# Optimization experiments

Hardware: AMD Instinct MI355X
Metric: run time of the kernel (lower is better)

The kernel has to match this reference:

```python
import jax, jax.numpy as jnp
from jax import lax
import numpy as np

GROUPS = 4


def _grid_sample_border(img, gx, gy):
    # img: [Bg, Cg, H, W]; gx, gy: [Bg, H, W] normalized grid in [-1, 1]
    # Replicates F.grid_sample(mode='bilinear', align_corners=False, padding_mode='border')
    Bg, Cg, H, W = img.shape
    ix = jnp.clip(((gx + 1.0) * W - 1.0) * 0.5, 0.0, W - 1.0)
    iy = jnp.clip(((gy + 1.0) * H - 1.0) * 0.5, 0.0, H - 1.0)
    x0 = jnp.floor(ix)
    y0 = jnp.floor(iy)
    wx = ix - x0
    wy = iy - y0
    x0i = x0.astype(jnp.int32)
    y0i = y0.astype(jnp.int32)
    x1i = jnp.minimum(x0i + 1, W - 1)
    y1i = jnp.minimum(y0i + 1, H - 1)

    def one(im, x0i, x1i, y0i, y1i, wx, wy):
        v00 = im[:, y0i, x0i]
        v01 = im[:, y0i, x1i]
        v10 = im[:, y1i, x0i]
        v11 = im[:, y1i, x1i]
        return (v00 * (1 - wx) * (1 - wy) + v01 * wx * (1 - wy)
                + v10 * (1 - wx) * wy + v11 * wx * wy)

    return jax.vmap(one)(img, x0i, x1i, y0i, y1i, wx, wy)


def setup_inputs() -> dict:
    key = jax.random.key(0)
    ks = jax.random.split(key, 8)
    B, N, C = 8, 4096, 768
    x = jax.random.normal(ks[0], (B, N, C), dtype=jnp.float32)
    dw_w = jax.random.normal(ks[1], (C, 1, 3, 3), dtype=jnp.float32) * 0.1  # depthwise kernel
    dw_b = jax.random.normal(ks[2], (C,), dtype=jnp.float32) * 0.1
    off_w = jax.random.normal(ks[3], (2 * GROUPS, C), dtype=jnp.float32) * 0.001  # std=0.001 init
    off_b = jnp.zeros((2 * GROUPS,), dtype=jnp.float32)
    wt_w = jax.random.normal(ks[4], (2 * GROUPS, C), dtype=jnp.float32) * 0.02
    wt_b = jnp.zeros((2 * GROUPS,), dtype=jnp.float32)
    offset_list = jnp.zeros((1,), dtype=jnp.int32)
    return {"x": x, "dw_w": dw_w, "dw_b": dw_b, "off_w": off_w, "off_b": off_b,
            "wt_w": wt_w, "wt_b": wt_b, "offset_list": offset_list,
            "patch_h": 64, "patch_w": 64}


def reference(x, dw_w, dw_b, off_w, off_b, wt_w, wt_b, offset_list, patch_h, patch_w):
    B, N, C = x.shape
    H, W = int(patch_h), int(patch_w)
    xi = jnp.transpose(x, (0, 2, 1)).reshape(B, C, H, W)

    # offset head: depthwise 3x3 conv -> GELU -> 1x1 conv to 2*groups channels
    dw = lax.conv_general_dilated(xi, dw_w, (1, 1), ((1, 1), (1, 1)),
                                  dimension_numbers=("NCHW", "OIHW", "NCHW"),
                                  feature_group_count=C)
    dw = jax.nn.gelu(dw + dw_b[None, :, None, None], approximate=False)
    off = jnp.einsum("bchw,oc->bohw", dw, off_w) + off_b[None, :, None, None]

    # weight head: 1x1 conv -> sigmoid
    wt = jax.nn.sigmoid(jnp.einsum("bchw,oc->bohw", xi, wt_w) + wt_b[None, :, None, None])

    off = (off * wt).reshape(B, 2, GROUPS, H, W)
    # fixed cross-shaped shifts: x-comp [0,0,-1,+1], y-comp [-1,+1,0,0]
    shifts = jnp.array([[0.0, 0.0, -1.0, 1.0], [-1.0, 1.0, 0.0, 0.0]],
                       dtype=x.dtype).reshape(1, 2, GROUPS, 1, 1)
    off = off + shifts

    cx = (jnp.arange(W, dtype=x.dtype) + 0.5)[None, None, None, :]  # pixel-center x coords
    cy = (jnp.arange(H, dtype=x.dtype) + 0.5)[None, None, :, None]  # pixel-center y coords
    gx = 2.0 * (cx + off[:, 0]) / W - 1.0  # [B, GROUPS, H, W]
    gy = 2.0 * (cy + off[:, 1]) / H - 1.0

    img = xi.reshape(B * GROUPS, C // GROUPS, H, W)
    samp = _grid_sample_border(img, gx.reshape(B * GROUPS, H, W),
                               gy.reshape(B * GROUPS, H, W))
    out = samp.reshape(B, C, N)
    return jnp.transpose(out, (0, 2, 1))  # [B, N, C]
```

## Files before the change

### kernel.cpp

```cpp
#include <hip/hip_runtime.h>
#include <math.h>

#define BB 8
#define CC 768
#define HH 64
#define WW 64
#define NN 4096
#define GG 4
#define NCHUNK 6
#define CHUNK 128

typedef __attribute__((ext_vector_type(8))) short short8;
typedef __attribute__((ext_vector_type(4))) float f32x4;

__device__ __forceinline__ unsigned short f2bf(float f) {
    union { float f; unsigned u; } v; v.f = f;
    unsigned r = v.u + 0x7FFFu + ((v.u >> 16) & 1u);
    return (unsigned short)(r >> 16);
}

__device__ __forceinline__ float gelu_fast(float v) {
    const float z = 1.5957691216f * v * fmaf(0.044715f, v * v, 1.0f);
    return __fdividef(v, 1.0f + __expf(-z));
}

__global__ __launch_bounds__(128, 4) void dq_conv_mfma(
    const float* __restrict__ x,
    const float* __restrict__ dw_w,
    const float* __restrict__ dw_b,
    const float* __restrict__ off_w,
    const float* __restrict__ wt_w,
    float* __restrict__ offpart)
{
    __shared__ unsigned short gl[16][144];
    __shared__ unsigned short xh[16][144];
    const int t = threadIdx.x;
    const int lane = t & 63, wv = t >> 6;
    const int xcd = blockIdx.x & 7;
    const int local = blockIdx.x >> 3;
    const int chunk = local % NCHUNK;
    const int r = xcd * (BB * HH / 8) + local / NCHUNK;
    const int h = r & (HH - 1);
    const int b = r >> 6;
    const int c = chunk * CHUNK + t;

    const int n = lane & 15, kg = lane >> 4;
    const float* wsrc = (wv == 0) ? off_w : wt_w;
    short8 bfrag[4];
#pragma unroll
    for (int kt = 0; kt < 4; ++kt) {
        const bool valid = (n < 8);
        const float* src = wsrc + (valid ? n : 0) * CC + chunk * CHUNK + kt * 32 + kg * 8;
        short8 bf;
#pragma unroll
        for (int j = 0; j < 8; ++j) {
            const float v = valid ? src[j] : 0.f;
            bf[j] = (short)f2bf(v);
        }
        bfrag[kt] = bf;
    }

    float w9[9];
#pragma unroll
    for (int j = 0; j < 9; ++j) w9[j] = dw_w[c * 9 + j];
    const float bias = dw_b[c];
    const bool tv = (h > 0), bv = (h < HH - 1);
    const float wt0 = tv ? w9[0] : 0.f, wt1 = tv ? w9[1] : 0.f, wt2 = tv ? w9[2] : 0.f;
    const float wb0 = bv ? w9[6] : 0.f, wb1 = bv ? w9[7] : 0.f, wb2 = bv ? w9[8] : 0.f;

    const float* base = x + (size_t)b * NN * CC + c;
    const float* rT = base + (size_t)((tv ? h - 1 : 0) * WW) * CC;
    const float* rM = base + (size_t)(h * WW) * CC;
    const float* rB = base + (size_t)((bv ? h + 1 : h) * WW) * CC;

    float cT[8], cM[8], cB[8], nT[8], nM[8], nB[8];
    float pT = 0.f, pM = 0.f, pB = 0.f;

#pragma unroll
    for (int j = 0; j < 8; ++j) {
        const size_t o = (size_t)j * CC;
        cT[j] = rT[o]; cM[j] = rM[o]; cB[j] = rB[o];
    }

#pragma unroll
    for (int q = 0; q < 4; ++q) {
#pragma unroll
        for (int hb = 0; hb < 2; ++hb) {
            const int wb = q * 2 + hb;
            if (wb < 7) {
#pragma unroll
                for (int j = 0; j < 8; ++j) {
                    const size_t o = (size_t)(wb * 8 + 8 + j) * CC;
                    nT[j] = rT[o]; nM[j] = rM[o]; nB[j] = rB[o];
                }
            } else {
#pragma unroll
                for (int j = 0; j < 8; ++j) { nT[j] = 0.f; nM[j] = 0.f; nB[j] = 0.f; }
            }
#pragma unroll
            for (int j = 0; j < 8; ++j) {
                const float lT = j ? cT[j - 1] : pT;
                const float lM = j ? cM[j - 1] : pM;
                const float lB = j ? cB[j - 1] : pB;
                const float rTv = (j == 7) ? nT[0] : cT[j + 1];
                const float rMv = (j == 7) ? nM[0] : cM[j + 1];
                const float rBv = (j == 7) ? nB[0] : cB[j + 1];
                const float conv = lT * wt0 + cT[j] * wt1 + rTv * wt2
                                 + lM * w9[3] + cM[j] * w9[4] + rMv * w9[5]
                                 + lB * wb0 + cB[j] * wb1 + rBv * wb2;
                const int colq = hb * 8 + j;
                gl[colq][t] = f2bf(gelu_fast(conv + bias));
                xh[colq][t] = f2bf(cM[j]);
            }
            pT = cT[7]; pM = cM[7]; pB = cB[7];
#pragma unroll
            for (int j = 0; j < 8; ++j) { cT[j] = nT[j]; cM[j] = nM[j]; cB[j] = nB[j]; }
        }

        __syncthreads();
        f32x4 acc = {0.f, 0.f, 0.f, 0.f};
        if (wv == 0) {
#pragma unroll
            for (int kt = 0; kt < 4; ++kt) {
                const short8 a = *(const short8*)&gl[n][kt * 32 + kg * 8];
                acc = __builtin_amdgcn_mfma_f32_16x16x32_bf16(a, bfrag[kt], acc, 0, 0, 0);
            }
        } else {
#pragma unroll
            for (int kt = 0; kt < 4; ++kt) {
                const short8 a = *(const short8*)&xh[n][kt * 32 + kg * 8];
                acc = __builtin_amdgcn_mfma_f32_16x16x32_bf16(a, bfrag[kt], acc, 0, 0, 0);
            }
        }
        if (n < 8) {
            const int plane = chunk * 16 + (wv ? 8 + n : n);
            const size_t gpos = (size_t)(b * NN) + h * WW + q * 16 + kg * 4;
            float4 st; st.x = acc[0]; st.y = acc[1]; st.z = acc[2]; st.w = acc[3];
            *(float4*)&offpart[(size_t)plane * (BB * NN) + gpos] = st;
        }
        if (q < 3) __syncthreads();
    }
}

__global__ __launch_bounds__(256) void dq_combine(
    const float* __restrict__ offpart,
    const float* __restrict__ off_b,
    const float* __restrict__ wt_b,
    float* __restrict__ ixiy)
{
    const int t = threadIdx.x;
    const int o = t >> 5;
    const int gpos = blockIdx.x * 32 + (t & 31);
    const int b = gpos >> 12;
    const int hw = gpos & 4095;
    const int h = hw >> 6, w = hw & 63;

    float so = 0.f, sw = 0.f;
#pragma unroll
    for (int ch = 0; ch < NCHUNK; ++ch) {
        so += offpart[((size_t)(ch * 16 + o)) * (BB * NN) + gpos];
        sw += offpart[((size_t)(ch * 16 + 8 + o)) * (BB * NN) + gpos];
    }
    const float sig = 1.f / (1.f + __expf(-(sw + wt_b[o])));
    const float val = (so + off_b[o]) * sig;

    if (o < 4) {
        const float shx = (o == 2) ? -1.f : ((o == 3) ? 1.f : 0.f);
        const float ix = fminf(fmaxf((float)w + val + shx, 0.f), (float)(WW - 1));
        ixiy[(b * GG + o) * NN + hw] = ix;
    } else {
        const int g = o - 4;
        const float shy = (g == 0) ? -1.f : ((g == 1) ? 1.f : 0.f);
        const float iy = fminf(fmaxf((float)h + val + shy, 0.f), (float)(HH - 1));
        ixiy[BB * GG * NN + (b * GG + g) * NN + hw] = iy;
    }
}

__global__ __launch_bounds__(192) void dq_sample_vec(
    const float* __restrict__ x,
    const float* __restrict__ ixiy,
    float* __restrict__ out)
{
    __shared__ float ixy[8];
    const int t = threadIdx.x;
    const int p = (blockIdx.x & 7) * (BB * NN / 8) + (blockIdx.x >> 3);
    const int b = p >> 12;
    const int hw = p & 4095;

    if (t < 8) {
        const int g = t & 3;
        const int plane = (t >> 2) * (BB * GG * NN);
        ixy[t] = ixiy[plane + (b * GG + g) * NN + hw];
    }
    __syncthreads();

    const int g = t / 48;
    const float ix = ixy[g], iy = ixy[4 + g];
    const float x0f = floorf(ix), y0f = floorf(iy);
    const float wx = ix - x0f, wy = iy - y0f;
    const int x0 = (int)x0f, y0 = (int)y0f;
    const int x1 = min(x0 + 1, WW - 1), y1 = min(y0 + 1, HH - 1);
    const int c4 = t * 4;
    const float* xb = x + (size_t)b * NN * CC;
    const float4 v00 = *(const float4*)(xb + (size_t)(y0 * WW + x0) * CC + c4);
    const float4 v01 = *(const float4*)(xb + (size_t)(y0 * WW + x1) * CC + c4);
    const float4 v10 = *(const float4*)(xb + (size_t)(y1 * WW + x0) * CC + c4);
    const float4 v11 = *(const float4*)(xb + (size_t)(y1 * WW + x1) * CC + c4);
    const float w00 = (1.f - wx) * (1.f - wy), w01 = wx * (1.f - wy);
    const float w10 = (1.f - wx) * wy,         w11 = wx * wy;
    float4 r;
    r.x = v00.x * w00 + v01.x * w01 + v10.x * w10 + v11.x * w11;
    r.y = v00.y * w00 + v01.y * w01 + v10.y * w10 + v11.y * w11;
    r.z = v00.z * w00 + v01.z * w01 + v10.z * w10 + v11.z * w11;
    r.w = v00.w * w00 + v01.w * w01 + v10.w * w10 + v11.w * w11;
    *(float4*)(out + (size_t)p * CC + c4) = r;
}

__global__ __launch_bounds__(256) void dqshift_offsets_kernel(
    const float* __restrict__ x, const float* __restrict__ dw_w,
    const float* __restrict__ dw_b, const float* __restrict__ off_w,
    const float* __restrict__ off_b, const float* __restrict__ wt_w,
    const float* __restrict__ wt_b, float* __restrict__ ixiy)
{
    const int wave = threadIdx.x >> 6;
    const int lane = threadIdx.x & 63;
    const int p = blockIdx.x * 4 + wave;
    const int b = p >> 12;
    const int hw = p & 4095;
    const int h = hw >> 6;
    const int w = hw & 63;
    const float* xb = x + (size_t)b * NN * CC;
    float accO[8], accW[8];
#pragma unroll
    for (int o = 0; o < 8; ++o) { accO[o] = 0.f; accW[o] = 0.f; }
    for (int k = 0; k < CC / 64; ++k) {
        const int c = lane + (k << 6);
        float conv = 0.f, xc = 0.f;
#pragma unroll
        for (int dy = -1; dy <= 1; ++dy) {
            const int hh = h + dy;
            const bool vy = (hh >= 0) && (hh < HH);
#pragma unroll
            for (int dx = -1; dx <= 1; ++dx) {
                const int ww = w + dx;
                const bool vv = vy && (ww >= 0) && (ww < WW);
                const float tt = vv ? xb[(size_t)(hh * WW + ww) * CC + c] : 0.f;
                if (dy == 0 && dx == 0) xc = tt;
                conv = fmaf(tt, dw_w[c * 9 + (dy + 1) * 3 + (dx + 1)], conv);
            }
        }
        const float gv = conv + dw_b[c];
        const float gle = 0.5f * gv * (1.0f + erff(gv * 0.70710678118654752f));
#pragma unroll
        for (int o = 0; o < 8; ++o) {
            accO[o] = fmaf(gle, off_w[o * CC + c], accO[o]);
            accW[o] = fmaf(xc, wt_w[o * CC + c], accW[o]);
        }
    }
#pragma unroll
    for (int o = 0; o < 8; ++o) {
#pragma unroll
        for (int s = 32; s > 0; s >>= 1) {
            accO[o] += __shfl_xor(accO[o], s, 64);
            accW[o] += __shfl_xor(accW[o], s, 64);
        }
    }
    if (lane == 0) {
        const float shx[4] = {0.f, 0.f, -1.f, 1.f};
        const float shy[4] = {-1.f, 1.f, 0.f, 0.f};
#pragma unroll
        for (int g = 0; g < 4; ++g) {
            const float sx = 1.f / (1.f + expf(-(accW[g] + wt_b[g])));
            const float sy = 1.f / (1.f + expf(-(accW[4 + g] + wt_b[4 + g])));
            const float ox = (accO[g] + off_b[g]) * sx + shx[g];
            const float oy = (accO[4 + g] + off_b[4 + g]) * sy + shy[g];
            const float ix = fminf(fmaxf((float)w + ox, 0.f), (float)(WW - 1));
            const float iy = fminf(fmaxf((float)h + oy, 0.f), (float)(HH - 1));
            const int idx = (b * GG + g) * NN + hw;
            ixiy[idx] = ix;
            ixiy[BB * GG * NN + idx] = iy;
        }
    }
}

__global__ __launch_bounds__(256) void dqshift_sample_kernel(
    const float* __restrict__ x,
    const float* __restrict__ ixiy,
    float* __restrict__ out)
{
    const int p = blockIdx.x;
    const int b = p >> 12;
    const int hw = p & 4095;
    const float* xb = x + (size_t)b * NN * CC;
    float* ob = out + (size_t)p * CC;

#pragma unroll
    for (int k = 0; k < 3; ++k) {
        const int c = threadIdx.x + (k << 8);
        const int g = c / (CC / GG);
        const int idx = (b * GG + g) * NN + hw;
        const float ix = ixiy[idx];
        const float iy = ixiy[BB * GG * NN + idx];
        const float x0f = floorf(ix);
        const float y0f = floorf(iy);
        const float wx = ix - x0f;
        const float wy = iy - y0f;
        const int x0 = (int)x0f;
        const int y0 = (int)y0f;
        const int x1 = min(x0 + 1, WW - 1);
        const int y1 = min(y0 + 1, HH - 1);
        const float* r0 = xb + (size_t)(y0 * WW) * CC + c;
        const float* r1 = xb + (size_t)(y1 * WW) * CC + c;
        const float v00 = r0[(size_t)x0 * CC];
        const float v01 = r0[(size_t)x1 * CC];
        const float v10 = r1[(size_t)x0 * CC];
        const float v11 = r1[(size_t)x1 * CC];
        ob[c] = v00 * (1.f - wx) * (1.f - wy) + v01 * wx * (1.f - wy)
              + v10 * (1.f - wx) * wy + v11 * wx * wy;
    }
}

extern "C" void kernel_launch(void* const* d_in, const int* in_sizes, int n_in,
                              void* d_out, int out_size, void* d_ws, size_t ws_size,
                              hipStream_t stream) {
    const float* x     = (const float*)d_in[0];
    const float* dw_w  = (const float*)d_in[1];
    const float* dw_b  = (const float*)d_in[2];
    const float* off_w = (const float*)d_in[3];
    const float* off_b = (const float*)d_in[4];
    const float* wt_w  = (const float*)d_in[5];
    const float* wt_b  = (const float*)d_in[6];

    float* ixiy = (float*)d_ws;
    float* offpart = (float*)d_ws + 2 * BB * GG * NN;
    const size_t need = (size_t)(2 * BB * GG * NN + NCHUNK * 16 * BB * NN) * 4;

    if (ws_size >= need) {
        dq_conv_mfma<<<BB * HH * NCHUNK, 128, 0, stream>>>(
            x, dw_w, dw_b, off_w, wt_w, offpart);
        dq_combine<<<BB * NN / 32, 256, 0, stream>>>(
            offpart, off_b, wt_b, ixiy);
        dq_sample_vec<<<BB * NN, 192, 0, stream>>>(
            x, ixiy, (float*)d_out);
    } else {
        dqshift_offsets_kernel<<<BB * NN / 4, 256, 0, stream>>>(
            x, dw_w, dw_b, off_w, off_b, wt_w, wt_b, ixiy);
        dqshift_sample_kernel<<<BB * NN, 256, 0, stream>>>(x, ixiy, (float*)d_out);
    }
}
```

Measured before the change: 76.18 us.

## Switch conv MFMA to fp16, double-buffer LDS, load x-head operands directly from global

Replaces bf16 software rounding with native fp16 conversion and uses the f16 MFMA instead. The weight-head wave now reads its A operands straight from global memory (cached, since the same rows were just loaded) rather than staging a second LDS array. The gelu staging buffer is double-buffered by q parity, so the trailing barrier per iteration is removed. This trades some precision range (fp16 vs bf16) and extra global reads for fewer LDS writes, fewer conversion instructions and one fewer barrier per step.

```diff
diff --git a/kernel.cpp b/kernel.cpp
--- a/kernel.cpp
+++ b/kernel.cpp
@@ -10,14 +10,8 @@
 #define NCHUNK 6
 #define CHUNK 128
 
-typedef __attribute__((ext_vector_type(8))) short short8;
+typedef __attribute__((ext_vector_type(8))) _Float16 half8;
 typedef __attribute__((ext_vector_type(4))) float f32x4;
-
-__device__ __forceinline__ unsigned short f2bf(float f) {
-    union { float f; unsigned u; } v; v.f = f;
-    unsigned r = v.u + 0x7FFFu + ((v.u >> 16) & 1u);
-    return (unsigned short)(r >> 16);
-}
 
 __device__ __forceinline__ float gelu_fast(float v) {
     const float z = 1.5957691216f * v * fmaf(0.044715f, v * v, 1.0f);
@@ -32,8 +26,7 @@
     const float* __restrict__ wt_w,
     float* __restrict__ offpart)
 {
-    __shared__ unsigned short gl[16][144];
-    __shared__ unsigned short xh[16][144];
+    __shared__ __attribute__((aligned(16))) _Float16 gl[2][16][144];
     const int t = threadIdx.x;
     const int lane = t & 63, wv = t >> 6;
     const int xcd = blockIdx.x & 7;
@@ -46,16 +39,16 @@
 
     const int n = lane & 15, kg = lane >> 4;
     const float* wsrc = (wv == 0) ? off_w : wt_w;
-    short8 bfrag[4];
+    half8 bfrag[4];
 #pragma unroll
     for (int kt = 0; kt < 4; ++kt) {
         const bool valid = (n < 8);
         const float* src = wsrc + (valid ? n : 0) * CC + chunk * CHUNK + kt * 32 + kg * 8;
-        short8 bf;
+        half8 bf;
 #pragma unroll
         for (int j = 0; j < 8; ++j) {
             const float v = valid ? src[j] : 0.f;
-            bf[j] = (short)f2bf(v);
+            bf[j] = (_Float16)v;
         }
         bfrag[kt] = bf;
     }
@@ -73,6 +66,8 @@
     const float* rM = base + (size_t)(h * WW) * CC;
     const float* rB = base + (size_t)((bv ? h + 1 : h) * WW) * CC;
 
+    const float* xq1 = x + ((size_t)(b * NN + h * WW + n)) * CC + chunk * CHUNK + kg * 8;
+
     float cT[8], cM[8], cB[8], nT[8], nM[8], nB[8];
     float pT = 0.f, pM = 0.f, pB = 0.f;
 
@@ -84,6 +79,7 @@
 
 #pragma unroll
     for (int q = 0; q < 4; ++q) {
+        const int qb = q & 1;
 #pragma unroll
         for (int hb = 0; hb < 2; ++hb) {
             const int wb = q * 2 + hb;
@@ -108,9 +104,7 @@
                 const float conv = lT * wt0 + cT[j] * wt1 + rTv * wt2
                                  + lM * w9[3] + cM[j] * w9[4] + rMv * w9[5]
                                  + lB * wb0 + cB[j] * wb1 + rBv * wb2;
-                const int colq = hb * 8 + j;
-                gl[colq][t] = f2bf(gelu_fast(conv + bias));
-                xh[colq][t] = f2bf(cM[j]);
+                gl[qb][hb * 8 + j][t] = (_Float16)gelu_fast(conv + bias);
             }
             pT = cT[7]; pM = cM[7]; pB = cB[7];
 #pragma unroll
@@ -122,14 +116,21 @@
         if (wv == 0) {
 #pragma unroll
             for (int kt = 0; kt < 4; ++kt) {
-                const short8 a = *(const short8*)&gl[n][kt * 32 + kg * 8];
-                acc = __builtin_amdgcn_mfma_f32_16x16x32_bf16(a, bfrag[kt], acc, 0, 0, 0);
+                const half8 a = *(const half8*)&gl[qb][n][kt * 32 + kg * 8];
+                acc = __builtin_amdgcn_mfma_f32_16x16x32_f16(a, bfrag[kt], acc, 0, 0, 0);
             }
         } else {
+            const float* xp = xq1 + (size_t)(q * 16) * CC;
 #pragma unroll
             for (int kt = 0; kt < 4; ++kt) {
-                const short8 a = *(const short8*)&xh[n][kt * 32 + kg * 8];
-                acc = __builtin_amdgcn_mfma_f32_16x16x32_bf16(a, bfrag[kt], acc, 0, 0, 0);
+                const float4 va = *(const float4*)(xp + kt * 32);
+                const float4 vb = *(const float4*)(xp + kt * 32 + 4);
+                half8 a;
+                a[0] = (_Float16)va.x; a[1] = (_Float16)va.y;
+                a[2] = (_Float16)va.z; a[3] = (_Float16)va.w;
+                a[4] = (_Float16)vb.x; a[5] = (_Float16)vb.y;
+                a[6] = (_Float16)vb.z; a[7] = (_Float16)vb.w;
+                acc = __builtin_amdgcn_mfma_f32_16x16x32_f16(a, bfrag[kt], acc, 0, 0, 0);
             }
         }
         if (n < 8) {
@@ -138,7 +139,6 @@
             float4 st; st.x = acc[0]; st.y = acc[1]; st.z = acc[2]; st.w = acc[3];
             *(float4*)&offpart[(size_t)plane * (BB * NN) + gpos] = st;
         }
-        if (q < 3) __syncthreads();
     }
 }
 
```

Result: slower. 82.52 us (+8.3%).
